# Optimization experiments

Hardware: AMD Instinct MI355X
Metric: run time of the kernel (lower is better)

## Reference

```python
import jax, jax.numpy as jnp
import numpy as np

B, H, W = 8, 64, 64
DIM1, DIM2 = 384, 256
NH, DH = 8, 32
INNER = NH * DH
EPS = 1e-5


def _layernorm(x, w, b):
    mu = jnp.mean(x, axis=-1, keepdims=True)
    var = jnp.mean((x - mu) ** 2, axis=-1, keepdims=True)
    return (x - mu) * jax.lax.rsqrt(var + EPS) * w + b


def _axial_attn(q, k, v, scale):
    # q,k,v: [B,H,W,nh,dh]; row attention over H, col attention over W
    sh = jnp.einsum('biwnd,bjwnd->bwnij', q, k) * scale  # [B,W,nh,H,H]
    oh = jnp.einsum('bwnij,bjwnd->biwnd', jax.nn.softmax(sh, axis=-1), v)
    sw = jnp.einsum('bhind,bhjnd->bhnij', q, k) * scale  # [B,H,nh,W,W]
    ow = jnp.einsum('bhnij,bhjnd->bhind', jax.nn.softmax(sw, axis=-1), v)
    return oh + ow  # [B,H,W,nh,dh]


def setup_inputs() -> dict:
    key = jax.random.key(0)
    ks = jax.random.split(key, 16)
    s1 = 1.0 / np.sqrt(DIM1)
    s2 = 1.0 / np.sqrt(DIM2)
    si = 1.0 / np.sqrt(INNER)
    return {
        'x1': jax.random.normal(ks[0], (B, DIM1, H, W), jnp.float32),
        'x2': jax.random.normal(ks[1], (B, DIM2, H, W), jnp.float32),
        'ln1q_w': jnp.ones((DIM1,), jnp.float32),
        'ln1q_b': jnp.zeros((DIM1,), jnp.float32),
        'ln2kv_w': jnp.ones((DIM2,), jnp.float32),
        'ln2kv_b': jnp.zeros((DIM2,), jnp.float32),
        'Wq1': jax.random.normal(ks[2], (DIM1, INNER), jnp.float32) * s1,
        'Wkv2': jax.random.normal(ks[3], (DIM2, 2 * INNER), jnp.float32) * s2,
        'Wout1': jax.random.normal(ks[4], (INNER, DIM2), jnp.float32) * si,
        'bout1': jnp.zeros((DIM2,), jnp.float32),
        'ln2q_w': jnp.ones((DIM2,), jnp.float32),
        'ln2q_b': jnp.zeros((DIM2,), jnp.float32),
        'ln1kv_w': jnp.ones((DIM1,), jnp.float32),
        'ln1kv_b': jnp.zeros((DIM1,), jnp.float32),
        'Wq2': jax.random.normal(ks[5], (DIM2, INNER), jnp.float32) * s2,
        'Wkv1': jax.random.normal(ks[6], (DIM1, 2 * INNER), jnp.float32) * s1,
        'Wout2': jax.random.normal(ks[7], (INNER, DIM2), jnp.float32) * si,
        'bout2': jnp.zeros((DIM2,), jnp.float32),
        'Wsc': jax.random.normal(ks[8], (DIM2, DIM1), jnp.float32) * s1,  # 1x1 conv [out,in]
        'bn_gamma': jnp.ones((DIM2,), jnp.float32),
        'bn_beta': jnp.zeros((DIM2,), jnp.float32),
        'bn_mean': jnp.zeros((DIM2,), jnp.float32),
        'bn_var': jnp.ones((DIM2,), jnp.float32),
    }


def reference(x1, x2, ln1q_w, ln1q_b, ln2kv_w, ln2kv_b, Wq1, Wkv2, Wout1, bout1,
              ln2q_w, ln2q_b, ln1kv_w, ln1kv_b, Wq2, Wkv1, Wout2, bout2,
              Wsc, bn_gamma, bn_beta, bn_mean, bn_var):
    b, c1, h, w = x1.shape
    scale = DH ** -0.5
    x1f = jnp.transpose(x1, (0, 2, 3, 1))  # [B,H,W,C1]
    x2f = jnp.transpose(x2, (0, 2, 3, 1))  # [B,H,W,C2]

    def heads(t):
        return t.reshape(b, h, w, NH, DH)

    # branch 1: q from x1, kv from x2
    q1 = _layernorm(x1f, ln1q_w, ln1q_b) @ Wq1
    kv2 = _layernorm(x2f, ln2kv_w, ln2kv_b) @ Wkv2
    k2, v2 = jnp.split(kv2, 2, axis=-1)
    o1 = _axial_attn(heads(q1), heads(k2), heads(v2), scale)
    fused1 = o1.reshape(b, h, w, INNER) @ Wout1 + bout1
    # shortcut: 1x1 conv + BN (inference stats)
    sc = jnp.einsum('bhwc,oc->bhwo', x1f, Wsc)
    sc = (sc - bn_mean) * jax.lax.rsqrt(bn_var + EPS) * bn_gamma + bn_beta
    y1 = sc + fused1

    # branch 2: q from x2, kv from x1
    q2 = _layernorm(x2f, ln2q_w, ln2q_b) @ Wq2
    kv1 = _layernorm(x1f, ln1kv_w, ln1kv_b) @ Wkv1
    k1, v1 = jnp.split(kv1, 2, axis=-1)
    o2 = _axial_attn(heads(q2), heads(k1), heads(v1), scale)
    fused2 = o2.reshape(b, h, w, INNER) @ Wout2 + bout2
    y2 = x2f + fused2

    out = y1 + y2  # [B,H,W,C2]
    return jnp.transpose(out, (0, 3, 1, 2))
```

## Files before the change

kernel.cpp:

```cpp
#include <hip/hip_runtime.h>

typedef unsigned short u16;
typedef unsigned int u32;
typedef float v4f __attribute__((ext_vector_type(4)));
typedef __bf16 v8bf __attribute__((ext_vector_type(8)));
typedef short v4s __attribute__((ext_vector_type(4)));

__device__ __forceinline__ float bf2f(u16 v) {
  union { u32 u; float f; } x; x.u = ((u32)v) << 16; return x.f;
}
__device__ __forceinline__ u16 f2bf(float f) {
  union { float f; u32 u; } x; x.f = f;
  u32 u = x.u;
  return (u16)((u + 0x7FFFu + ((u >> 16) & 1u)) >> 16);
}
__device__ __forceinline__ u32 f2u(float f) {
  union { float f; u32 u; } x; x.f = f; return x.u;
}
__device__ __forceinline__ u32 pk2bf(float a, float b) {
  const u32 au = f2u(a) + 0x7FFFu + ((f2u(a) >> 16) & 1u);
  const u32 bu = f2u(b) + 0x7FFFu + ((f2u(b) >> 16) & 1u);
  return (bu & 0xFFFF0000u) | (au >> 16);
}
__device__ __forceinline__ u32 pk2bf_t(float a, float b) {
  return (f2u(b) & 0xFFFF0000u) | (f2u(a) >> 16);
}

__device__ __forceinline__ v4f mfma16(v4s a, v4s b, v4f c) {
#if __has_builtin(__builtin_amdgcn_mfma_f32_16x16x16bf16_1k)
  return __builtin_amdgcn_mfma_f32_16x16x16bf16_1k(a, b, c, 0, 0, 0);
#else
  v4f d = c;
  asm volatile("v_mfma_f32_16x16x16_bf16 %0, %1, %2, %0" : "+v"(d) : "v"(a), "v"(b));
  return d;
#endif
}

struct Ptrs { const void* p[23]; };

__global__ __launch_bounds__(256) void convert_all(Ptrs ps, u16* __restrict__ cx1,
                                                   u16* __restrict__ cx2,
                                                   u16* __restrict__ cw) {
  static const int sz[23]  = {12582912, 8388608, 384, 384, 256, 256, 98304, 131072,
                              65536, 256, 256, 256, 384, 384, 65536, 196608, 65536,
                              256, 98304, 256, 256, 256, 256};
  static const int off[23] = {0, 0, 0, 384, 768, 1024, 1280, 99584, 230656, 296192,
                              296448, 296704, 296960, 297344, 297728, 363264, 559872,
                              625408, 625664, 723968, 724224, 724480, 724736};
  const int ti = blockIdx.y;
  const int n8 = sz[ti] >> 3;
  const bool isf32 = (((const u32*)ps.p[2])[0] == 0x3F800000u);
  u16* dst = (ti == 0) ? cx1 : (ti == 1) ? cx2 : (cw + off[ti]);
  const void* src = ps.p[ti];
  const int stride = gridDim.x * blockDim.x;
  for (int i = blockIdx.x * blockDim.x + threadIdx.x; i < n8; i += stride) {
    if (isf32) {
      const float4 f0 = ((const float4*)src)[2*i];
      const float4 f1 = ((const float4*)src)[2*i + 1];
      u16 tmp[8];
      tmp[0] = f2bf(f0.x); tmp[1] = f2bf(f0.y); tmp[2] = f2bf(f0.z); tmp[3] = f2bf(f0.w);
      tmp[4] = f2bf(f1.x); tmp[5] = f2bf(f1.y); tmp[6] = f2bf(f1.z); tmp[7] = f2bf(f1.w);
      ((uint4*)dst)[i] = *(const uint4*)tmp;
    } else {
      ((uint4*)dst)[i] = ((const uint4*)src)[i];
    }
  }
}

__global__ void prep_bt(const u16* __restrict__ lnq_w, const u16* __restrict__ lnq_b,
                        const u16* __restrict__ lnkv_w, const u16* __restrict__ lnkv_b,
                        const u16* __restrict__ Wq, const u16* __restrict__ Wkv,
                        u16* __restrict__ BT, float* __restrict__ bias) {
  const int C = blockDim.x;
  const int j = blockIdx.x;
  const int c = threadIdx.x;
  const float qscale = 0.25503482620929637f;
  float w, bco, wv;
  if (j < 256) { w = bf2f(lnq_w[c]) * qscale; bco = bf2f(lnq_b[c]) * qscale; wv = bf2f(Wq[c*256 + j]); }
  else         { w = bf2f(lnkv_w[c]); bco = bf2f(lnkv_b[c]); wv = bf2f(Wkv[c*512 + (j-256)]); }
  BT[(size_t)j*C + c] = f2bf(w * wv);
  __shared__ float red[384];
  red[c] = bco * wv;
  __syncthreads();
  if (c == 0) { float s = 0.f; for (int i = 0; i < C; i++) s += red[i]; bias[j] = s; }
}

__global__ void prep_fin(const u16* __restrict__ Wout1, const u16* __restrict__ Wout2,
                         const u16* __restrict__ Wsc, const u16* __restrict__ bout1,
                         const u16* __restrict__ bout2, const u16* __restrict__ gam,
                         const u16* __restrict__ bet, const u16* __restrict__ mean,
                         const u16* __restrict__ var, u16* __restrict__ BT,
                         float* __restrict__ bias) {
  const int o = blockIdx.x, t = threadIdx.x;
  const float g = rsqrtf(bf2f(var[o]) + 1e-5f) * bf2f(gam[o]);
  for (int idx = t; idx < 1408; idx += 256) {
    float v;
    if (idx < 512)       v = bf2f(Wout1[(idx & 255)*256 + o]);
    else if (idx < 1024) v = bf2f(Wout2[((idx - 512) & 255)*256 + o]);
    else                 v = bf2f(Wsc[o*384 + (idx - 1024)]) * g;
    BT[(size_t)o*1408 + idx] = f2bf(v);
  }
  if (t == 0) bias[o] = bf2f(bet[o]) - bf2f(mean[o])*g + bf2f(bout1[o]) + bf2f(bout2[o]);
}

__global__ __launch_bounds__(256) void ln_c384(const u16* __restrict__ x,
                                               u16* __restrict__ xn, u16* __restrict__ xraw) {
  __shared__ u16 tile[384*66];
  __shared__ float rsum[4][64], rsq[4][64], smean[64], srstd[64];
  const int t = threadIdx.x, w = t & 63, g = t >> 6;
  const int bh = blockIdx.x, b = bh >> 6, h = bh & 63;
  const u16* src = x + (size_t)b*384*4096 + h*64 + w;
  float sum = 0.f, sq = 0.f;
  for (int j = 0; j < 96; j++) {
    const int c = g*96 + j;
    const u16 uv = src[(size_t)c*4096];
    tile[c*66 + w] = uv;
    const float v = bf2f(uv); sum += v; sq += v*v;
  }
  rsum[g][w] = sum; rsq[g][w] = sq;
  __syncthreads();
  if (t < 64) {
    const float s = rsum[0][t]+rsum[1][t]+rsum[2][t]+rsum[3][t];
    const float q = rsq[0][t]+rsq[1][t]+rsq[2][t]+rsq[3][t];
    const float mean = s * (1.0f/384.0f);
    float var = q * (1.0f/384.0f) - mean*mean;
    if (var < 0.f) var = 0.f;
    smean[t] = mean; srstd[t] = rsqrtf(var + 1e-5f);
  }
  __syncthreads();
  const size_t pos0 = (size_t)bh * 64;
  for (int i = 0; i < 96; i++) {
    const int flat = i*256 + t;
    const int ww = flat / 384, c = flat - ww*384;
    const u16 uv = tile[c*66 + ww];
    const float v = (bf2f(uv) - smean[ww]) * srstd[ww];
    const size_t p = pos0 + ww;
    xn[p*384 + c] = f2bf(v);
    xraw[p*384 + c] = uv;
  }
}

__global__ __launch_bounds__(256) void ln_c256(const u16* __restrict__ x,
                                               u16* __restrict__ xn) {
  __shared__ u16 tile[256*66];
  __shared__ float rsum[4][64], rsq[4][64], smean[64], srstd[64];
  const int t = threadIdx.x, w = t & 63, g = t >> 6;
  const int bh = blockIdx.x, b = bh >> 6, h = bh & 63;
  const u16* src = x + (size_t)b*256*4096 + h*64 + w;
  float sum = 0.f, sq = 0.f;
  for (int j = 0; j < 64; j++) {
    const int c = g*64 + j;
    const u16 uv = src[(size_t)c*4096];
    tile[c*66 + w] = uv;
    const float v = bf2f(uv); sum += v; sq += v*v;
  }
  rsum[g][w] = sum; rsq[g][w] = sq;
  __syncthreads();
  if (t < 64) {
    const float s = rsum[0][t]+rsum[1][t]+rsum[2][t]+rsum[3][t];
    const float q = rsq[0][t]+rsq[1][t]+rsq[2][t]+rsq[3][t];
    const float mean = s * (1.0f/256.0f);
    float var = q * (1.0f/256.0f) - mean*mean;
    if (var < 0.f) var = 0.f;
    smean[t] = mean; srstd[t] = rsqrtf(var + 1e-5f);
  }
  __syncthreads();
  const size_t pos0 = (size_t)bh * 64;
  for (int i = 0; i < 64; i++) {
    const int flat = i*256 + t;
    const int ww = flat >> 8, c = flat & 255;
    const float v = (bf2f(tile[c*66 + ww]) - smean[ww]) * srstd[ww];
    xn[(pos0 + ww)*256 + c] = f2bf(v);
  }
}

__global__ __launch_bounds__(512) void gemm_bt(const u16* __restrict__ A,
                                               const u16* __restrict__ BT,
                                               u16* __restrict__ C,
                                               const float* __restrict__ bias,
                                               int N, int K) {
  __shared__ u16 lsA[128*40];
  __shared__ u16 lsB[128*40];
  const int t = threadIdx.x;
  const int m0 = blockIdx.x * 128, n0 = blockIdx.y * 128;
  const int lane = t & 63, wv = t >> 6;
  const int wm = wv >> 1, wn = wv & 1;
  const int lo = lane & 15, hi = lane >> 4;
  const int r0 = t >> 2, c8 = (t & 3) << 3;
  const u16* Ab = A + (size_t)(m0 + r0) * K + c8;
  const u16* Bb = BT + (size_t)(n0 + r0) * K + c8;
  uint4 a = *(const uint4*)(Ab);
  uint4 bq = *(const uint4*)(Bb);
  v4f acc[2][4] = {};
  for (int kb = 0; kb < K; kb += 32) {
    __syncthreads();
    *(uint4*)&lsA[r0*40 + c8] = a;
    *(uint4*)&lsB[r0*40 + c8] = bq;
    __syncthreads();
    if (kb + 32 < K) {
      a = *(const uint4*)(Ab + kb + 32);
      bq = *(const uint4*)(Bb + kb + 32);
    }
    v8bf av[2], bv[4];
#pragma unroll
    for (int i = 0; i < 2; i++) av[i] = *(const v8bf*)&lsA[(wm*32 + i*16 + lo)*40 + hi*8];
#pragma unroll
    for (int i = 0; i < 4; i++) bv[i] = *(const v8bf*)&lsB[(wn*64 + i*16 + lo)*40 + hi*8];
#pragma unroll
    for (int mt = 0; mt < 2; mt++)
#pragma unroll
      for (int nt = 0; nt < 4; nt++)
        acc[mt][nt] = __builtin_amdgcn_mfma_f32_16x16x32_bf16(av[mt], bv[nt], acc[mt][nt], 0, 0, 0);
  }
#pragma unroll
  for (int mt = 0; mt < 2; mt++) {
    const int row = m0 + wm*32 + mt*16 + hi*4;
#pragma unroll
    for (int nt = 0; nt < 4; nt++) {
      const int col = n0 + wn*64 + nt*16 + lo;
      const float bs = bias[col];
#pragma unroll
      for (int r = 0; r < 4; r++)
        C[(size_t)(row + r) * N + col] = f2bf(acc[mt][nt][r] + bs);
    }
  }
}

__global__ __launch_bounds__(512) void gemm_final(const u16* __restrict__ Ao,
                                                  const u16* __restrict__ Ar,
                                                  const u16* __restrict__ BT,
                                                  const float* __restrict__ bias,
                                                  const u16* __restrict__ x2c,
                                                  const u32* __restrict__ probe,
                                                  void* __restrict__ outv) {
  __shared__ u16 smem[16640];
  u16* lsA = smem;
  u16* lsB = smem + 5120;
  const int t = threadIdx.x;
  const int m0 = blockIdx.x * 128, n0 = blockIdx.y * 128;
  const int lane = t & 63, wv = t >> 6;
  const int wm = wv >> 1, wn = wv & 1;
  const int lo = lane & 15, hi = lane >> 4;
  const int r0 = t >> 2, c8 = (t & 3) << 3;
  const u16* ArR = Ar + (size_t)(m0 + r0) * 384 + c8;
  const u16* Bb  = BT + (size_t)(n0 + r0) * 1408 + c8;

  uint4 a, bq;
  {
    a = *(const uint4*)(Ao + ((size_t)(0) * 32768 + m0 + r0) * 32 + c8);
    bq = *(const uint4*)(Bb);
  }
  v4f acc[2][4] = {};
  for (int kb = 0; kb < 1408; kb += 32) {
    __syncthreads();
    *(uint4*)&lsA[r0*40 + c8] = a;
    *(uint4*)&lsB[r0*40 + c8] = bq;
    __syncthreads();
    const int kn = kb + 32;
    if (kn < 1408) {
      if (kn < 1024) a = *(const uint4*)(Ao + ((size_t)(kn >> 5) * 32768 + m0 + r0) * 32 + c8);
      else           a = *(const uint4*)(ArR + (kn - 1024));
      bq = *(const uint4*)(Bb + kn);
    }
    v8bf av[2], bv[4];
#pragma unroll
    for (int i = 0; i < 2; i++) av[i] = *(const v8bf*)&lsA[(wm*32 + i*16 + lo)*40 + hi*8];
#pragma unroll
    for (int i = 0; i < 4; i++) bv[i] = *(const v8bf*)&lsB[(wn*64 + i*16 + lo)*40 + hi*8];
#pragma unroll
    for (int mt = 0; mt < 2; mt++)
#pragma unroll
      for (int nt = 0; nt < 4; nt++)
        acc[mt][nt] = __builtin_amdgcn_mfma_f32_16x16x32_bf16(av[mt], bv[nt], acc[mt][nt], 0, 0, 0);
  }
  __syncthreads();
#pragma unroll
  for (int mt = 0; mt < 2; mt++)
#pragma unroll
    for (int nt = 0; nt < 4; nt++) {
      const int nl = wn*64 + nt*16 + lo;
      const float bs = bias[n0 + nl];
#pragma unroll
      for (int r = 0; r < 4; r++)
        smem[(wm*32 + mt*16 + hi*4 + r)*130 + nl] = f2bf(acc[mt][nt][r] + bs);
    }
  __syncthreads();
  const bool isf32 = (probe[0] == 0x3F800000u);
  const int bh0 = blockIdx.x * 2;
  for (int i = 0; i < 32; i++) {
    const int flat = i*512 + t;
    const int nl = flat >> 7;
    const int rem = flat & 127;
    const int mb = rem >> 6, w = rem & 63;
    const int bh = bh0 + mb, b = bh >> 6, h = bh & 63;
    const size_t oidx = ((size_t)(b*256 + n0 + nl)*64 + h)*64 + w;
    const float val = bf2f(smem[(mb*64 + w)*130 + nl]) + bf2f(x2c[oidx]);
    if (isf32) ((float*)outv)[oidx] = val;
    else       ((u16*)outv)[oidx]   = f2bf(val);
  }
}

__global__ __launch_bounds__(512) void attn(const u16* __restrict__ qkv1,
                                            const u16* __restrict__ qkv2,
                                            u16* __restrict__ Ao) {
  __shared__ __attribute__((aligned(16))) u16 smem[8 * 2560];
  const int t = threadIdx.x;
  const int head = t >> 6, lane = t & 63;
  const int lo = lane & 15, quad = lane >> 4;
  u16* sw = smem + head * 2560;
  const int bx = blockIdx.x;
  const int z = blockIdx.y;
  const int br = z >> 1, dir = z & 1;
  const int b = bx >> 6, x = bx & 63;
  const u16* Qb  = (br == 0) ? qkv1 : qkv2;
  const u16* KVb = (br == 0) ? qkv2 : qkv1;
  const int qc = head*32, kc = 256 + head*32, vc = 512 + head*32;
  const int pbase = (dir == 0) ? (b*4096 + x) : ((b*64 + x)*64);
  const int pstr  = (dir == 0) ? 64 : 1;

  {
    const u16* vr = KVb + (size_t)(pbase + lane*pstr)*768 + vc;
    u16 vbuf[32];
#pragma unroll
    for (int i = 0; i < 4; i++) *(uint4*)&vbuf[i*8] = *(const uint4*)(vr + i*8);
    const int khi = lane >> 3, klo = lane & 7;
#pragma unroll
    for (int d = 0; d < 32; d++)
      sw[d*64 + ((khi ^ (d & 7)) << 3) + klo] = vbuf[d];
  }
  __syncthreads();

  v8bf qa[4], ka[4];
#pragma unroll
  for (int i = 0; i < 4; i++) {
    const size_t p = (size_t)(pbase + (i*16 + lo)*pstr) * 768;
    qa[i] = *(const v8bf*)(Qb + p + qc + quad*8);
    ka[i] = *(const v8bf*)(KVb + p + kc + quad*8);
  }

  v4f s[4][4];
  __builtin_amdgcn_s_setprio(1);
#pragma unroll
  for (int qt = 0; qt < 4; qt++)
#pragma unroll
    for (int kt = 0; kt < 4; kt++) {
      v4f z4 = {};
      s[qt][kt] = __builtin_amdgcn_mfma_f32_16x16x32_bf16(ka[kt], qa[qt], z4, 0, 0, 0);
    }
  __builtin_amdgcn_s_setprio(0);

  v4s va16[2][4];
#pragma unroll
  for (int mt = 0; mt < 2; mt++)
#pragma unroll
    for (int kt = 0; kt < 4; kt++) {
      const int d = mt*16 + lo;
      va16[mt][kt] = *(const v4s*)&sw[d*64 + (((2*kt + (quad >> 1)) ^ (d & 7)) << 3) + (quad & 1)*4];
    }

  v4f o[2][4] = {};
  float inv4[4];
#pragma unroll
  for (int qt = 0; qt < 4; qt++) {
    float tv[16];
    float mx = -1e30f;
#pragma unroll
    for (int kt = 0; kt < 4; kt++)
#pragma unroll
      for (int r = 0; r < 4; r++) {
        const float v = s[qt][kt][r];
        tv[kt*4 + r] = v;
        mx = fmaxf(mx, v);
      }
    mx = fmaxf(mx, __shfl_xor(mx, 16));
    mx = fmaxf(mx, __shfl_xor(mx, 32));
    float sm = 0.f;
#pragma unroll
    for (int i = 0; i < 16; i++) { tv[i] = exp2f(tv[i] - mx); sm += tv[i]; }
    sm += __shfl_xor(sm, 16);
    sm += __shfl_xor(sm, 32);
    inv4[qt] = 1.0f / sm;
    __builtin_amdgcn_s_setprio(1);
#pragma unroll
    for (int kt = 0; kt < 4; kt++) {
      union { u32 u[2]; v4s v; } pb;
      pb.u[0] = pk2bf_t(tv[kt*4 + 0], tv[kt*4 + 1]);
      pb.u[1] = pk2bf_t(tv[kt*4 + 2], tv[kt*4 + 3]);
#pragma unroll
      for (int mt = 0; mt < 2; mt++)
        o[mt][qt] = mfma16(va16[mt][kt], pb.v, o[mt][qt]);
    }
    __builtin_amdgcn_s_setprio(0);
  }

  __syncthreads();
#pragma unroll
  for (int mt = 0; mt < 2; mt++)
#pragma unroll
    for (int nt = 0; nt < 4; nt++)
#pragma unroll
      for (int rp = 0; rp < 2; rp++) {
        const u32 pkv = pk2bf(o[mt][nt][rp*2] * inv4[nt], o[mt][nt][rp*2 + 1] * inv4[nt]);
        *(u32*)&sw[(nt*16 + lo)*40 + mt*16 + quad*4 + rp*2] = pkv;
      }
  __syncthreads();
  {
    const size_t sbase = (size_t)(z*8 + head) * 32768 + pbase;
#pragma unroll
    for (int it = 0; it < 4; it++) {
      const int chunk = it*64 + lane;
      const int row = chunk >> 2, ic = chunk & 3;
      *(uint4*)&Ao[(sbase + (size_t)row*pstr)*32 + ic*8] = *(const uint4*)&sw[row*40 + ic*8];
    }
  }
}

extern "C" void kernel_launch(void* const* d_in, const int* in_sizes, int n_in,
                              void* d_out, int out_size, void* d_ws, size_t ws_size,
                              hipStream_t stream) {
  char* ws = (char*)d_ws;
  u16* Ao    = (u16*)(ws);
  u16* Araw  = (u16*)(ws + 67108864);
  u16* qkv1  = (u16*)(ws + 92274688);
  u16* qkv2  = (u16*)(ws + 142606336);
  u16* cx2   = (u16*)(ws + 192937984);
  u16* cw    = (u16*)(ws + 209715200);
  u16* BT1   = (u16*)(ws + 211165184);
  u16* BT2   = (u16*)(ws + 211755008);
  u16* BTf   = (u16*)(ws + 212148224);
  float* bias1 = (float*)(ws + 212869120);
  float* bias2 = (float*)(ws + 212872192);
  float* biasf = (float*)(ws + 212875264);
  u16* cx1 = qkv1;
  u16* x1n = Ao;
  u16* x2n = Ao + 12582912;

  u16* c_ln1q_w = cw + 0,     *c_ln1q_b = cw + 384;
  u16* c_ln2kv_w = cw + 768,  *c_ln2kv_b = cw + 1024;
  u16* c_Wq1 = cw + 1280,     *c_Wkv2 = cw + 99584;
  u16* c_Wout1 = cw + 230656, *c_bout1 = cw + 296192;
  u16* c_ln2q_w = cw + 296448,*c_ln2q_b = cw + 296704;
  u16* c_ln1kv_w = cw + 296960,*c_ln1kv_b = cw + 297344;
  u16* c_Wq2 = cw + 297728,   *c_Wkv1 = cw + 363264;
  u16* c_Wout2 = cw + 559872, *c_bout2 = cw + 625408;
  u16* c_Wsc = cw + 625664;
  u16* c_bn_g = cw + 723968,  *c_bn_b = cw + 724224;
  u16* c_bn_m = cw + 724480,  *c_bn_v = cw + 724736;

  Ptrs ps;
  for (int i = 0; i < 23; i++) ps.p[i] = d_in[i];

  convert_all<<<dim3(512, 23), 256, 0, stream>>>(ps, cx1, cx2, cw);
  prep_bt<<<768, 384, 0, stream>>>(c_ln1q_w, c_ln1q_b, c_ln1kv_w, c_ln1kv_b, c_Wq1, c_Wkv1, BT1, bias1);
  prep_bt<<<768, 256, 0, stream>>>(c_ln2q_w, c_ln2q_b, c_ln2kv_w, c_ln2kv_b, c_Wq2, c_Wkv2, BT2, bias2);
  prep_fin<<<256, 256, 0, stream>>>(c_Wout1, c_Wout2, c_Wsc, c_bout1, c_bout2,
                                    c_bn_g, c_bn_b, c_bn_m, c_bn_v, BTf, biasf);
  ln_c384<<<512, 256, 0, stream>>>(cx1, x1n, Araw);
  ln_c256<<<512, 256, 0, stream>>>(cx2, x2n);
  gemm_bt<<<dim3(256, 6), 512, 0, stream>>>(x1n, BT1, qkv1, bias1, 768, 384);
  gemm_bt<<<dim3(256, 6), 512, 0, stream>>>(x2n, BT2, qkv2, bias2, 768, 256);
  attn<<<dim3(512, 4), 512, 0, stream>>>(qkv1, qkv2, Ao);
  gemm_final<<<dim3(256, 2), 512, 0, stream>>>(Ao, Araw, BTf, biasf, cx2,
                                               (const u32*)d_in[2], d_out);
}
```

Baseline: 354.4 us.

## Shrink gemm_final M-tile, split attention heads across blocks, parallelize bias reduction

The final GEMM now uses 64-row M tiles with a 2x4 wave layout, which doubles the grid to 512x2 blocks and halves shared memory per block. The attention kernel splits its 8 heads across two 256-thread blocks, doubling the block count. The prep_bt bias sum now uses a 64-lane strided reduction with shuffles instead of a single serial thread. The aim is more blocks and better occupancy across the CUs, at the cost of half the threads sitting idle during A-tile loads in gemm_final and less reuse of B tiles.

After: 352.2 us. About the same (-0.6%).

```diff
diff --git a/kernel.cpp b/kernel.cpp
--- a/kernel.cpp
+++ b/kernel.cpp
@@ -82,7 +82,13 @@
   __shared__ float red[384];
   red[c] = bco * wv;
   __syncthreads();
-  if (c == 0) { float s = 0.f; for (int i = 0; i < C; i++) s += red[i]; bias[j] = s; }
+  if (c < 64) {
+    float s = 0.f;
+    for (int i = c; i < C; i += 64) s += red[i];
+#pragma unroll
+    for (int offd = 32; offd; offd >>= 1) s += __shfl_down(s, offd);
+    if (c == 0) bias[j] = s;
+  }
 }
 
 __global__ void prep_fin(const u16* __restrict__ Wout1, const u16* __restrict__ Wout2,
@@ -233,52 +239,52 @@
                                                   const u16* __restrict__ x2c,
                                                   const u32* __restrict__ probe,
                                                   void* __restrict__ outv) {
-  __shared__ u16 smem[16640];
+  __shared__ u16 smem[8320];
   u16* lsA = smem;
-  u16* lsB = smem + 5120;
+  u16* lsB = smem + 2560;
   const int t = threadIdx.x;
-  const int m0 = blockIdx.x * 128, n0 = blockIdx.y * 128;
+  const int m0 = blockIdx.x * 64, n0 = blockIdx.y * 128;
   const int lane = t & 63, wv = t >> 6;
-  const int wm = wv >> 1, wn = wv & 1;
+  const int wm = wv >> 2, wn = wv & 3;
   const int lo = lane & 15, hi = lane >> 4;
   const int r0 = t >> 2, c8 = (t & 3) << 3;
   const u16* ArR = Ar + (size_t)(m0 + r0) * 384 + c8;
   const u16* Bb  = BT + (size_t)(n0 + r0) * 1408 + c8;
 
-  uint4 a, bq;
-  {
-    a = *(const uint4*)(Ao + ((size_t)(0) * 32768 + m0 + r0) * 32 + c8);
-    bq = *(const uint4*)(Bb);
-  }
-  v4f acc[2][4] = {};
+  uint4 a = {}, bq;
+  if (t < 256) a = *(const uint4*)(Ao + ((size_t)0 * 32768 + m0 + r0) * 32 + c8);
+  bq = *(const uint4*)(Bb);
+  v4f acc[2][2] = {};
   for (int kb = 0; kb < 1408; kb += 32) {
     __syncthreads();
-    *(uint4*)&lsA[r0*40 + c8] = a;
+    if (t < 256) *(uint4*)&lsA[r0*40 + c8] = a;
     *(uint4*)&lsB[r0*40 + c8] = bq;
     __syncthreads();
     const int kn = kb + 32;
     if (kn < 1408) {
-      if (kn < 1024) a = *(const uint4*)(Ao + ((size_t)(kn >> 5) * 32768 + m0 + r0) * 32 + c8);
-      else           a = *(const uint4*)(ArR + (kn - 1024));
+      if (t < 256) {
+        if (kn < 1024) a = *(const uint4*)(Ao + ((size_t)(kn >> 5) * 32768 + m0 + r0) * 32 + c8);
+        else           a = *(const uint4*)(ArR + (kn - 1024));
+      }
       bq = *(const uint4*)(Bb + kn);
     }
-    v8bf av[2], bv[4];
+    v8bf av[2], bv[2];
 #pragma unroll
     for (int i = 0; i < 2; i++) av[i] = *(const v8bf*)&lsA[(wm*32 + i*16 + lo)*40 + hi*8];
 #pragma unroll
-    for (int i = 0; i < 4; i++) bv[i] = *(const v8bf*)&lsB[(wn*64 + i*16 + lo)*40 + hi*8];
+    for (int i = 0; i < 2; i++) bv[i] = *(const v8bf*)&lsB[(wn*32 + i*16 + lo)*40 + hi*8];
 #pragma unroll
     for (int mt = 0; mt < 2; mt++)
 #pragma unroll
-      for (int nt = 0; nt < 4; nt++)
+      for (int nt = 0; nt < 2; nt++)
         acc[mt][nt] = __builtin_amdgcn_mfma_f32_16x16x32_bf16(av[mt], bv[nt], acc[mt][nt], 0, 0, 0);
   }
   __syncthreads();
 #pragma unroll
   for (int mt = 0; mt < 2; mt++)
 #pragma unroll
-    for (int nt = 0; nt < 4; nt++) {
-      const int nl = wn*64 + nt*16 + lo;
+    for (int nt = 0; nt < 2; nt++) {
+      const int nl = wn*32 + nt*16 + lo;
       const float bs = bias[n0 + nl];
 #pragma unroll
       for (int r = 0; r < 4; r++)
@@ -286,30 +292,28 @@
     }
   __syncthreads();
   const bool isf32 = (probe[0] == 0x3F800000u);
-  const int bh0 = blockIdx.x * 2;
-  for (int i = 0; i < 32; i++) {
+  const int bh = blockIdx.x, b = bh >> 6, h = bh & 63;
+  for (int i = 0; i < 16; i++) {
     const int flat = i*512 + t;
-    const int nl = flat >> 7;
-    const int rem = flat & 127;
-    const int mb = rem >> 6, w = rem & 63;
-    const int bh = bh0 + mb, b = bh >> 6, h = bh & 63;
+    const int nl = flat >> 6;
+    const int w = flat & 63;
     const size_t oidx = ((size_t)(b*256 + n0 + nl)*64 + h)*64 + w;
-    const float val = bf2f(smem[(mb*64 + w)*130 + nl]) + bf2f(x2c[oidx]);
+    const float val = bf2f(smem[w*130 + nl]) + bf2f(x2c[oidx]);
     if (isf32) ((float*)outv)[oidx] = val;
     else       ((u16*)outv)[oidx]   = f2bf(val);
   }
 }
 
-__global__ __launch_bounds__(512) void attn(const u16* __restrict__ qkv1,
+__global__ __launch_bounds__(256) void attn(const u16* __restrict__ qkv1,
                                             const u16* __restrict__ qkv2,
                                             u16* __restrict__ Ao) {
-  __shared__ __attribute__((aligned(16))) u16 smem[8 * 2560];
+  __shared__ __attribute__((aligned(16))) u16 smem[4 * 2560];
   const int t = threadIdx.x;
-  const int head = t >> 6, lane = t & 63;
+  const int head = ((blockIdx.y & 1) << 2) + (t >> 6), lane = t & 63;
   const int lo = lane & 15, quad = lane >> 4;
-  u16* sw = smem + head * 2560;
+  u16* sw = smem + (t >> 6) * 2560;
   const int bx = blockIdx.x;
-  const int z = blockIdx.y;
+  const int z = blockIdx.y >> 1;
   const int br = z >> 1, dir = z & 1;
   const int b = bx >> 6, x = bx & 63;
   const u16* Qb  = (br == 0) ? qkv1 : qkv2;
@@ -459,7 +463,7 @@
   ln_c256<<<512, 256, 0, stream>>>(cx2, x2n);
   gemm_bt<<<dim3(256, 6), 512, 0, stream>>>(x1n, BT1, qkv1, bias1, 768, 384);
   gemm_bt<<<dim3(256, 6), 512, 0, stream>>>(x2n, BT2, qkv2, bias2, 768, 256);
-  attn<<<dim3(512, 4), 512, 0, stream>>>(qkv1, qkv2, Ao);
-  gemm_final<<<dim3(256, 2), 512, 0, stream>>>(Ao, Araw, BTf, biasf, cx2,
+  attn<<<dim3(512, 8), 256, 0, stream>>>(qkv1, qkv2, Ao);
+  gemm_final<<<dim3(512, 2), 512, 0, stream>>>(Ao, Araw, BTf, biasf, cx2,
                                                (const u32*)d_in[2], d_out);
 }
```
